# Optimization experiments

Hardware: AMD Instinct MI355X
Metric: run time of the kernel (lower is better)

The kernel has to match this reference:

```python
import jax, jax.numpy as jnp
import numpy as np
import math

B, L, S, T = 16, 256, 128, 128
Q_DIM, F_DIM, H_DIM, OUT_DIM = 512, 512, 512, 512


def setup_inputs() -> dict:
    key = jax.random.key(0)
    ks = jax.random.split(key, 10)
    inp = {
        "query": jax.random.normal(ks[0], (B, L, Q_DIM), dtype=jnp.float32),
        "src": jax.random.normal(ks[1], (B, S, F_DIM), dtype=jnp.float32),
        "trg": jax.random.normal(ks[2], (B, T, F_DIM), dtype=jnp.float32),
        # LinearAct params (Linear + identity act; out layer uses tanh)
        "Wq": jax.random.normal(ks[3], (Q_DIM, H_DIM), dtype=jnp.float32) / math.sqrt(Q_DIM),
        "bq": jnp.zeros((H_DIM,), dtype=jnp.float32),
        "Ws": jax.random.normal(ks[4], (F_DIM, H_DIM), dtype=jnp.float32) / math.sqrt(F_DIM),
        "bs": jnp.zeros((H_DIM,), dtype=jnp.float32),
        "Wt": jax.random.normal(ks[5], (F_DIM, H_DIM), dtype=jnp.float32) / math.sqrt(F_DIM),
        "bt": jnp.zeros((H_DIM,), dtype=jnp.float32),
        "Wo": jax.random.normal(ks[6], (2 * H_DIM + Q_DIM, OUT_DIM), dtype=jnp.float32) / math.sqrt(2 * H_DIM + Q_DIM),
        "bo": jnp.zeros((OUT_DIM,), dtype=jnp.float32),
    }
    return inp


def reference(query, src, trg, Wq, bq, Ws, bs, Wt, bt, Wo, bo):
    b, l, _ = query.shape
    _, s, f = src.shape
    _, t, _ = trg.shape
    hid_dim = Wq.shape[1]

    q = query @ Wq + bq                              # b, l, h
    # pad one all-zero feature row onto src and trg (as in torch.cat with pad_tensor)
    pad = jnp.zeros((b, 1, f), dtype=src.dtype)
    src_p = jnp.concatenate([src, pad], axis=1)       # b, s+1, f
    trg_p = jnp.concatenate([trg, pad], axis=1)       # b, t+1, f
    s_key = src_p @ Ws + bs                           # b, s+1, h
    t_key = trg_p @ Wt + bt                           # b, t+1, h

    # trilinear scores: b, l, s+1, t+1
    weight = jnp.einsum('blk,bsk,btk->blst', q, s_key, t_key) / math.sqrt(hid_dim)
    # joint softmax over the flattened (s+1)*(t+1) axis
    weight = jax.nn.softmax(weight.reshape(b, l, -1), axis=-1).reshape(b, l, s + 1, t + 1)

    s_ctx = jnp.einsum('blst,bsk->blk', weight, s_key)  # b, l, h
    t_ctx = jnp.einsum('blst,btk->blk', weight, t_key)  # b, l, h

    x = jnp.concatenate([query, s_ctx, t_ctx], axis=-1)  # b, l, q+2h
    return jnp.tanh(x @ Wo + bo)
```

## Files before the change

### kernel.cpp

```cpp
#include <hip/hip_runtime.h>
#include <math.h>

#define HD 512
#define SP 129
#define RPAD 144
#define WPAD 160
#define NBATCH 16
#define MQ 4096
#define SCALE 0.04419417382415922f
#define SCLG2E 0.06375871645788f
#define TANH2E 2.8853900817779268f

typedef _Float16 f16;
typedef _Float16 f16x8 __attribute__((ext_vector_type(8)));
typedef _Float16 f16x4 __attribute__((ext_vector_type(4)));
typedef float f32x4  __attribute__((ext_vector_type(4)));

__device__ __forceinline__ void gload_lds16(const f16* g, f16* l) {
  __builtin_amdgcn_global_load_lds(
      (const __attribute__((address_space(1))) void*)g,
      (__attribute__((address_space(3))) void*)l, 16, 0, 0);
}

__global__ __launch_bounds__(256) void prep_kernel(
    const float* __restrict__ Wq, const float* __restrict__ Ws,
    const float* __restrict__ Wt, const float* __restrict__ Wo,
    const float* __restrict__ bs, const float* __restrict__ bt,
    f16* __restrict__ WqT, f16* __restrict__ WsT,
    f16* __restrict__ WtT, f16* __restrict__ WoT,
    f16* __restrict__ skey, f16* __restrict__ tkey,
    f16* __restrict__ skeyT, f16* __restrict__ tkeyT)
{
  const int id = blockIdx.x;
  const int tid = threadIdx.x;
  if (id >= 384) {
    int i = (id - 384) * 256 + tid;
    int b = i >> 9, n = i & 511;
    for (int r = 128; r < RPAD; ++r) {
      skey[((size_t)b*RPAD + r)*HD + n] = (r == 128) ? (f16)bs[n] : (f16)0.f;
      tkey[((size_t)b*RPAD + r)*HD + n] = (r == 128) ? (f16)bt[n] : (f16)0.f;
    }
    size_t o = ((size_t)b*512 + n)*WPAD;
    for (int c = 128; c < WPAD; ++c) {
      skeyT[o + c] = (c == 128) ? (f16)bs[n] : (f16)0.f;
      tkeyT[o + c] = (c == 128) ? (f16)bt[n] : (f16)0.f;
    }
    return;
  }
  const float* W; f16* WT; int K; int rest;
  if (id < 64)       { W = Wq; WT = WqT; K = 512;  rest = id; }
  else if (id < 128) { W = Ws; WT = WsT; K = 512;  rest = id - 64; }
  else if (id < 192) { W = Wt; WT = WtT; K = 512;  rest = id - 128; }
  else               { W = Wo; WT = WoT; K = 1536; rest = id - 192; }
  const int k0 = (rest >> 3) * 64, n0 = (rest & 7) * 64;

  __shared__ float t[64][65];
  const int r = tid >> 4, c4 = (tid & 15) * 4;
  #pragma unroll
  for (int i = 0; i < 4; ++i) {
    int k = r + 16*i;
    float4 v = *(const float4*)(W + (size_t)(k0 + k)*512 + n0 + c4);
    t[k][c4] = v.x; t[k][c4+1] = v.y; t[k][c4+2] = v.z; t[k][c4+3] = v.w;
  }
  __syncthreads();
  #pragma unroll
  for (int i = 0; i < 4; ++i) {
    int n = r + 16*i;
    f16x4 v = { (f16)t[c4][n], (f16)t[c4+1][n], (f16)t[c4+2][n], (f16)t[c4+3][n] };
    *(f16x4*)(WT + (size_t)(n0 + n)*K + k0 + c4) = v;
  }
}

__global__ __launch_bounds__(256) void gemm_in(
    const float* __restrict__ query, const float* __restrict__ src,
    const float* __restrict__ trg,
    const f16* __restrict__ WqT, const f16* __restrict__ WsT,
    const f16* __restrict__ WtT,
    const float* __restrict__ bq, const float* __restrict__ bsv,
    const float* __restrict__ btv,
    f16* __restrict__ q_h, f16* __restrict__ skey, f16* __restrict__ tkey,
    f16* __restrict__ skeyT, f16* __restrict__ tkeyT)
{
  __shared__ __align__(16) f16 As[64*64];
  __shared__ __align__(16) f16 Bs[64*64];
  const int x = blockIdx.x;
  const float* A; const f16* WT; const float* bias; int bm; int iskey;
  f16 *Ch, *CT;
  if (x < 64)      { A = query; WT = WqT; bias = bq;  bm = x*64;      iskey = 0; Ch = q_h;  CT = nullptr; }
  else if (x < 96) { A = src;   WT = WsT; bias = bsv; bm = (x-64)*64; iskey = 1; Ch = skey; CT = skeyT; }
  else             { A = trg;   WT = WtT; bias = btv; bm = (x-96)*64; iskey = 1; Ch = tkey; CT = tkeyT; }
  const int bn = blockIdx.y * 64;
  const int tid  = threadIdx.x;
  const int lane = tid & 63;
  const int w    = tid >> 6;
  const int wr   = w & 1, wc = w >> 1;
  const int fq   = lane >> 4, fr = lane & 15;

  f32x4 acc[2][2] = {};

  for (int k0 = 0; k0 < 512; k0 += 64) {
    #pragma unroll
    for (int i = 0; i < 2; ++i) {
      int idx = tid + 256*i;
      int r = idx >> 3, c = idx & 7;
      const float* ap = A + (size_t)(bm + r)*512 + k0 + c*8;
      float4 x0 = *(const float4*)ap;
      float4 x1 = *(const float4*)(ap + 4);
      f16x8 va = { (f16)x0.x, (f16)x0.y, (f16)x0.z, (f16)x0.w,
                   (f16)x1.x, (f16)x1.y, (f16)x1.z, (f16)x1.w };
      const uint4 vb = *(const uint4*)(WT + (size_t)(bn + r)*512 + k0 + c*8);
      int o = ((r << 7) + (c << 4)) ^ ((r & 7) << 4);
      *(f16x8*)((char*)As + o) = va;
      *(uint4*)((char*)Bs + o) = vb;
    }
    __syncthreads();
    #pragma unroll
    for (int ks = 0; ks < 2; ++ks) {
      f16x8 af[2], bf_[2];
      #pragma unroll
      for (int i = 0; i < 2; ++i) {
        int ra = wr*32 + i*16 + fr;
        int oa = ((ra << 7) + (ks << 6) + (fq << 4)) ^ ((ra & 7) << 4);
        af[i] = *(const f16x8*)((const char*)As + oa);
        int rb = wc*32 + i*16 + fr;
        int ob = ((rb << 7) + (ks << 6) + (fq << 4)) ^ ((rb & 7) << 4);
        bf_[i] = *(const f16x8*)((const char*)Bs + ob);
      }
      #pragma unroll
      for (int i = 0; i < 2; ++i)
        #pragma unroll
        for (int j = 0; j < 2; ++j)
          acc[i][j] = __builtin_amdgcn_mfma_f32_16x16x32_f16(af[i], bf_[j], acc[i][j], 0, 0, 0);
    }
    __syncthreads();
  }

  #pragma unroll
  for (int i = 0; i < 2; ++i) {
    #pragma unroll
    for (int j = 0; j < 2; ++j) {
      int n = bn + wc*32 + j*16 + fr;
      float bv = bias[n];
      if (iskey) {
        const int m0 = bm + wr*32 + i*16 + fq*4;
        f16 vals[4];
        #pragma unroll
        for (int r = 0; r < 4; ++r) {
          int m = m0 + r;
          f16 xx = (f16)(acc[i][j][r] + bv);
          vals[r] = xx;
          int mo = (m >> 7) * RPAD + (m & 127);
          Ch[(size_t)mo*512 + n] = xx;
        }
        f16x4 v4 = { vals[0], vals[1], vals[2], vals[3] };
        *(f16x4*)(CT + ((size_t)(m0 >> 7)*512 + n)*WPAD + (m0 & 127)) = v4;
      } else {
        #pragma unroll
        for (int r = 0; r < 4; ++r) {
          int m = bm + wr*32 + i*16 + fq*4 + r;
          Ch[(size_t)m*512 + n] = (f16)(acc[i][j][r] + bv);
        }
      }
    }
  }
}

__global__ __launch_bounds__(256) void border_kernel(
    const f16* __restrict__ q_h, const f16* __restrict__ skey,
    const f16* __restrict__ tkey, float* __restrict__ Sb)
{
  const int blk = blockIdx.x;
  const int b  = blk >> 4;
  const int z  = (blk >> 3) & 1;
  const int mt = (blk >> 1) & 3;
  const int jh = blk & 1;
  const int j0 = jh ? 5 : 0;
  const int nj = jh ? 4 : 5;
  const int tasks = nj * 64;
  const f16* keys = (z ? skey : tkey) + ((size_t)b*RPAD + j0*16)*HD;
  const f16* u    = (z ? tkey : skey) + ((size_t)b*RPAD + 128)*HD;
  const int gid0 = b*256 + mt*64;

  __shared__ __align__(16) f16 Ks[80*32];
  const int tid = threadIdx.x, lane = tid & 63, w = tid >> 6;
  const int fq = lane >> 4, fr = lane & 15;
  const int rslot = (fq ^ ((fr >> 1) & 3)) * 8;

  f32x4 acc[5] = {};

  for (int kt = 0; kt < 16; ++kt) {
    uint4 t0, t1;
    {
      int r0 = tid >> 2, c0 = tid & 3;
      t0 = *(const uint4*)(keys + (size_t)r0*HD + kt*32 + c0*8);
      if (tid + 256 < tasks) {
        int r1 = (tid + 256) >> 2;
        t1 = *(const uint4*)(keys + (size_t)r1*HD + kt*32 + c0*8);
      }
    }
    __syncthreads();
    {
      int r0 = tid >> 2, c0 = tid & 3;
      int ws0 = (c0 ^ ((r0 >> 1) & 3)) * 8;
      *(uint4*)(&Ks[r0*32 + ws0]) = t0;
      if (tid + 256 < tasks) {
        int r1 = (tid + 256) >> 2;
        int ws1 = (c0 ^ ((r1 >> 1) & 3)) * 8;
        *(uint4*)(&Ks[r1*32 + ws1]) = t1;
      }
    }
    __syncthreads();
    const f16x8 qf = *(const f16x8*)(q_h + (size_t)(gid0 + w*16 + fr)*HD + kt*32 + fq*8);
    const f16x8 uv = *(const f16x8*)(u + kt*32 + fq*8);
    const f16x8 a = qf * uv;
    #pragma unroll
    for (int j = 0; j < 5; ++j) {
      if (j < nj) {
        const f16x8 bfr = *(const f16x8*)(&Ks[(j*16 + fr)*32 + rslot]);
        acc[j] = __builtin_amdgcn_mfma_f32_16x16x32_f16(a, bfr, acc[j], 0, 0, 0);
      }
    }
  }

  float* dst = Sb + (size_t)z*MQ*RPAD;
  #pragma unroll
  for (int j = 0; j < 5; ++j)
    if (j < nj) {
      #pragma unroll
      for (int r = 0; r < 4; ++r)
        dst[(size_t)(gid0 + w*16 + fq*4 + r)*RPAD + (j0 + j)*16 + fr] = acc[j][r];
    }
}

__global__ __launch_bounds__(256, 4) void attn_core(
    const f16* __restrict__ qg,
    const f16* __restrict__ skey,
    const f16* __restrict__ tkey,
    const float* __restrict__ Sb,
    f16* __restrict__ wsn,
    f16* __restrict__ wtn)
{
  __shared__ __align__(16) f16 KB[2*2*128*32];
  __shared__ __align__(16) f16 qs[HD];
  __shared__ float wsA[2][128];
  __shared__ float wtA[2][128];
  __shared__ float redA[4], redB[4], redC[4], redD[4], redE[4];
  __shared__ float cornerP;

  const int tid  = threadIdx.x;
  const int lane = tid & 63;
  const int w    = tid >> 6;
  const int rb   = w & 1;
  const int cb   = w >> 1;
  const int fq   = lane >> 4;
  const int fr   = lane & 15;
  const int so   = (fq ^ ((fr >> 1) & 3)) << 3;
  const int gc   = ((lane & 3) ^ ((lane >> 3) & 3)) * 8;

  const int gid = ((int)blockIdx.x & 7) * 512 + ((int)blockIdx.x >> 3);
  const int b   = gid >> 8;
  const f16* skg = skey + (size_t)b * RPAD * HD;
  const f16* tkg = tkey + (size_t)b * RPAD * HD;

  if (tid < 64) *(uint4*)(qs + tid*8) = *(const uint4*)(qg + (size_t)gid*HD + tid*8);

  auto stage = [&](int kt, int buf) {
    #pragma unroll
    for (int n = 0; n < 4; ++n) {
      int idx = w*4 + n;
      int key = idx >> 3;
      int rg  = idx & 7;
      const f16* g = (key ? tkg : skg)
                   + (size_t)(rg*16 + (lane >> 2))*HD + kt*32 + gc;
      f16* l = &KB[((buf*2 + key)*128 + rg*16)*32];
      gload_lds16(g, l);
    }
  };

  f32x4 acc[4][4] = {};

  auto mfma_kt = [&](int kt, int cur) {
    const f16x8 qv = *(const f16x8*)(&qs[kt*32 + fq*8]);
    const int abase = (cur*2 + 0)*128*32;
    const int bbase = (cur*2 + 1)*128*32;
    f16x8 B[4];
    #pragma unroll
    for (int j = 0; j < 4; ++j) {
      int rt = cb*64 + j*16 + fr;
      B[j] = *(const f16x8*)(&KB[bbase + rt*32 + so]);
    }
    __builtin_amdgcn_s_setprio(1);
    #pragma unroll
    for (int i = 0; i < 4; ++i) {
      int rs = rb*64 + i*16 + fr;
      const f16x8 raw = *(const f16x8*)(&KB[abase + rs*32 + so]);
      const f16x8 a = raw * qv;
      #pragma unroll
      for (int j = 0; j < 4; ++j)
        acc[i][j] = __builtin_amdgcn_mfma_f32_16x16x32_f16(a, B[j], acc[i][j], 0, 0, 0);
    }
    __builtin_amdgcn_s_setprio(0);
  };

  stage(0, 0);
  __syncthreads();

  for (int kt = 0; kt < 16; ++kt) {
    const int cur = kt & 1;
    if (kt < 15) {
      stage(kt + 1, cur ^ 1);
      asm volatile("s_waitcnt vmcnt(4)" ::: "memory");
    } else {
      asm volatile("s_waitcnt vmcnt(0)" ::: "memory");
    }
    __builtin_amdgcn_s_barrier();
    mfma_kt(kt, cur);
    __builtin_amdgcn_s_barrier();
  }

  float m = -3e38f;
  #pragma unroll
  for (int i = 0; i < 4; ++i)
    #pragma unroll
    for (int j = 0; j < 4; ++j)
      #pragma unroll
      for (int r = 0; r < 4; ++r) m = fmaxf(m, acc[i][j][r]);
  #pragma unroll
  for (int off = 32; off > 0; off >>= 1) m = fmaxf(m, __shfl_xor(m, off));
  if (lane == 0) redA[w] = m;

  const float* SbT = Sb + (size_t)gid*RPAD;
  const float* SbS = Sb + (size_t)MQ*RPAD + (size_t)gid*RPAD;
  const float btv = (tid < 129) ? SbT[tid] : -3e38f;
  const float bsv = (tid < 128) ? SbS[tid] : -3e38f;
  float bm = fmaxf(btv, bsv);
  #pragma unroll
  for (int off = 32; off > 0; off >>= 1) bm = fmaxf(bm, __shfl_xor(bm, off));
  if (lane == 0) redB[w] = bm;
  __syncthreads();
  const float mraw = fmaxf(
      fmaxf(fmaxf(redA[0], redA[1]), fmaxf(redA[2], redA[3])),
      fmaxf(fmaxf(redB[0], redB[1]), fmaxf(redB[2], redB[3])));

  float csum = 0.f;
  #pragma unroll
  for (int i = 0; i < 4; ++i)
    #pragma unroll
    for (int j = 0; j < 4; ++j)
      #pragma unroll
      for (int r = 0; r < 4; ++r) {
        float p = exp2f((acc[i][j][r] - mraw) * SCLG2E);
        acc[i][j][r] = p;
        csum += p;
      }
  #pragma unroll
  for (int off = 32; off > 0; off >>= 1) csum += __shfl_xor(csum, off);
  if (lane == 0) redC[w] = csum;

  #pragma unroll
  for (int i = 0; i < 4; ++i) {
    #pragma unroll
    for (int r = 0; r < 4; ++r) {
      float rs = acc[i][0][r] + acc[i][1][r] + acc[i][2][r] + acc[i][3][r];
      rs += __shfl_xor(rs, 1); rs += __shfl_xor(rs, 2);
      rs += __shfl_xor(rs, 4); rs += __shfl_xor(rs, 8);
      if (fr == 0) wsA[cb][rb*64 + i*16 + fq*4 + r] = rs;
    }
  }
  #pragma unroll
  for (int j = 0; j < 4; ++j) {
    float cs = 0.f;
    #pragma unroll
    for (int i = 0; i < 4; ++i)
      #pragma unroll
      for (int r = 0; r < 4; ++r) cs += acc[i][j][r];
    cs += __shfl_xor(cs, 16); cs += __shfl_xor(cs, 32);
    if (fq == 0) wtA[rb][cb*64 + j*16 + fr] = cs;
  }

  const float pbt = (tid < 129) ? exp2f((btv - mraw) * SCLG2E) : 0.f;
  const float pbs = (tid < 128) ? exp2f((bsv - mraw) * SCLG2E) : 0.f;
  float sbt = pbt, sbs = pbs;
  #pragma unroll
  for (int off = 32; off > 0; off >>= 1) {
    sbt += __shfl_xor(sbt, off);
    sbs += __shfl_xor(sbs, off);
  }
  if (lane == 0) { redD[w] = sbt; redE[w] = sbs; }
  if (tid == 128) cornerP = pbt;
  __syncthreads();

  const float pbt_sum = redD[0] + redD[1] + redD[2] + redD[3];
  const float pbs_sum = redE[0] + redE[1] + redE[2] + redE[3];
  const float core_sum = redC[0] + redC[1] + redC[2] + redC[3];
  const float invZ = 1.0f / (core_sum + pbt_sum + pbs_sum);

  if (tid < WPAD) {
    float wsv = (tid < 128) ? (wsA[0][tid] + wsA[1][tid] + pbs)
              : (tid == 128) ? pbt_sum : 0.f;
    float wtv = (tid < 128) ? (wtA[0][tid] + wtA[1][tid] + pbt)
              : (tid == 128) ? (pbs_sum + cornerP) : 0.f;
    wsn[(size_t)gid*WPAD + tid] = (f16)(wsv * invZ);
    wtn[(size_t)gid*WPAD + tid] = (f16)(wtv * invZ);
  }
}

__global__ __launch_bounds__(256) void ctx_gemm(
    const f16* __restrict__ wsn, const f16* __restrict__ wtn,
    const f16* __restrict__ skeyT, const f16* __restrict__ tkeyT,
    f16* __restrict__ sctx, f16* __restrict__ tctx)
{
  __shared__ __align__(16) f16 As[64*168];
  __shared__ __align__(16) f16 Bs[64*168];
  const int z = blockIdx.x & 1, b = blockIdx.x >> 1;
  const int mt = blockIdx.y, nt = blockIdx.z;
  const int tid = threadIdx.x, lane = tid & 63, w = tid >> 6;
  const int wr = w & 1, wc = w >> 1;
  const int fq = lane >> 4, fr = lane & 15;

  const f16* A  = (z ? wtn : wsn) + ((size_t)b*256 + mt*64)*WPAD;
  const f16* Bt = (z ? tkeyT : skeyT) + ((size_t)b*512 + nt*64)*WPAD;

  for (int t = tid; t < 1280; t += 256) {
    int r = t / 20, c = t % 20;
    *(uint4*)(&As[r*168 + c*8]) = *(const uint4*)(A + (size_t)r*WPAD + c*8);
    *(uint4*)(&Bs[r*168 + c*8]) = *(const uint4*)(Bt + (size_t)r*WPAD + c*8);
  }
  __syncthreads();

  f32x4 acc[2][2] = {};
  #pragma unroll
  for (int ks = 0; ks < 5; ++ks) {
    f16x8 af[2], bf_[2];
    #pragma unroll
    for (int i = 0; i < 2; ++i) {
      af[i]  = *(const f16x8*)(&As[(wr*32 + i*16 + fr)*168 + ks*32 + fq*8]);
      bf_[i] = *(const f16x8*)(&Bs[(wc*32 + i*16 + fr)*168 + ks*32 + fq*8]);
    }
    #pragma unroll
    for (int i = 0; i < 2; ++i)
      #pragma unroll
      for (int j = 0; j < 2; ++j)
        acc[i][j] = __builtin_amdgcn_mfma_f32_16x16x32_f16(af[i], bf_[j], acc[i][j], 0, 0, 0);
  }

  f16* out = z ? tctx : sctx;
  #pragma unroll
  for (int i = 0; i < 2; ++i)
    #pragma unroll
    for (int j = 0; j < 2; ++j) {
      int col = nt*64 + wc*32 + j*16 + fr;
      #pragma unroll
      for (int r = 0; r < 4; ++r) {
        int row = b*256 + mt*64 + wr*32 + i*16 + fq*4 + r;
        out[(size_t)row*HD + col] = (f16)acc[i][j][r];
      }
    }
}

__global__ __launch_bounds__(256) void gemm_out(
    const float* __restrict__ query, const f16* __restrict__ sctx,
    const f16* __restrict__ tctx, const f16* __restrict__ WoT,
    const float* __restrict__ bias, float* __restrict__ C)
{
  __shared__ __align__(16) f16 As[64*64];
  __shared__ __align__(16) f16 Bs[64*64];
  const int tid  = threadIdx.x;
  const int lane = tid & 63;
  const int w    = tid >> 6;
  const int wr   = w & 1, wc = w >> 1;
  const int fq   = lane >> 4, fr = lane & 15;
  const int bm = blockIdx.x * 64, bn = blockIdx.y * 64;

  f32x4 acc[2][2] = {};

  for (int k0 = 0; k0 < 1536; k0 += 64) {
    const int seg  = k0 >> 9;
    const int kloc = k0 & 511;
    #pragma unroll
    for (int i = 0; i < 2; ++i) {
      int idx = tid + 256*i;
      int r = idx >> 3, c = idx & 7;
      int o = ((r << 7) + (c << 4)) ^ ((r & 7) << 4);
      if (seg == 0) {
        const float* ap = query + (size_t)(bm + r)*512 + kloc + c*8;
        float4 x0 = *(const float4*)ap;
        float4 x1 = *(const float4*)(ap + 4);
        f16x8 va = { (f16)x0.x, (f16)x0.y, (f16)x0.z, (f16)x0.w,
                     (f16)x1.x, (f16)x1.y, (f16)x1.z, (f16)x1.w };
        *(f16x8*)((char*)As + o) = va;
      } else {
        const f16* Ap = (seg == 1) ? sctx : tctx;
        *(uint4*)((char*)As + o) = *(const uint4*)(Ap + (size_t)(bm + r)*512 + kloc + c*8);
      }
      *(uint4*)((char*)Bs + o) = *(const uint4*)(WoT + (size_t)(bn + r)*1536 + k0 + c*8);
    }
    __syncthreads();
    #pragma unroll
    for (int ks = 0; ks < 2; ++ks) {
      f16x8 af[2], bf_[2];
      #pragma unroll
      for (int i = 0; i < 2; ++i) {
        int ra = wr*32 + i*16 + fr;
        int oa = ((ra << 7) + (ks << 6) + (fq << 4)) ^ ((ra & 7) << 4);
        af[i] = *(const f16x8*)((const char*)As + oa);
        int rb = wc*32 + i*16 + fr;
        int ob = ((rb << 7) + (ks << 6) + (fq << 4)) ^ ((rb & 7) << 4);
        bf_[i] = *(const f16x8*)((const char*)Bs + ob);
      }
      #pragma unroll
      for (int i = 0; i < 2; ++i)
        #pragma unroll
        for (int j = 0; j < 2; ++j)
          acc[i][j] = __builtin_amdgcn_mfma_f32_16x16x32_f16(af[i], bf_[j], acc[i][j], 0, 0, 0);
    }
    __syncthreads();
  }

  #pragma unroll
  for (int i = 0; i < 2; ++i)
    #pragma unroll
    for (int j = 0; j < 2; ++j) {
      int n = bn + wc*32 + j*16 + fr;
      float bv = bias[n];
      #pragma unroll
      for (int r = 0; r < 4; ++r) {
        int m = bm + wr*32 + i*16 + fq*4 + r;
        float xx = acc[i][j][r] + bv;
        xx = fminf(fmaxf(xx, -20.f), 20.f);
        float e = exp2f(TANH2E * xx);
        C[(size_t)m*HD + n] = (e - 1.0f) / (e + 1.0f);
      }
    }
}

extern "C" void kernel_launch(void* const* d_in, const int* in_sizes, int n_in,
                              void* d_out, int out_size, void* d_ws, size_t ws_size,
                              hipStream_t stream) {
  (void)in_sizes; (void)n_in; (void)out_size; (void)ws_size;
  const float* query = (const float*)d_in[0];
  const float* src   = (const float*)d_in[1];
  const float* trg   = (const float*)d_in[2];
  const float* Wq    = (const float*)d_in[3];
  const float* bq    = (const float*)d_in[4];
  const float* Wsm   = (const float*)d_in[5];
  const float* bs    = (const float*)d_in[6];
  const float* Wtm   = (const float*)d_in[7];
  const float* bt    = (const float*)d_in[8];
  const float* Wo    = (const float*)d_in[9];
  const float* bo    = (const float*)d_in[10];
  float* out = (float*)d_out;

  char* p = (char*)d_ws;
  f16* WqT   = (f16*)p;  p += (size_t)HD*HD*2;
  f16* WsT   = (f16*)p;  p += (size_t)HD*HD*2;
  f16* WtT   = (f16*)p;  p += (size_t)HD*HD*2;
  f16* WoT   = (f16*)p;  p += (size_t)1536*HD*2;
  f16* q_h   = (f16*)p;  p += (size_t)MQ*HD*2;
  f16* skey  = (f16*)p;  p += (size_t)NBATCH*RPAD*HD*2;
  f16* tkey  = (f16*)p;  p += (size_t)NBATCH*RPAD*HD*2;
  f16* skeyT = (f16*)p;  p += (size_t)NBATCH*HD*WPAD*2;
  f16* tkeyT = (f16*)p;  p += (size_t)NBATCH*HD*WPAD*2;
  f16* wsn   = (f16*)p;  p += (size_t)MQ*WPAD*2;
  f16* wtn   = (f16*)p;  p += (size_t)MQ*WPAD*2;
  f16* sctx  = (f16*)p;  p += (size_t)MQ*HD*2;
  f16* tctx  = (f16*)p;  p += (size_t)MQ*HD*2;
  float* Sb  = (float*)p; p += (size_t)2*MQ*RPAD*4;

  dim3 blk(256);
  prep_kernel<<<dim3(416), blk, 0, stream>>>(Wq, Wsm, Wtm, Wo, bs, bt,
                                             WqT, WsT, WtT, WoT,
                                             skey, tkey, skeyT, tkeyT);
  gemm_in<<<dim3(128, 8), blk, 0, stream>>>(query, src, trg, WqT, WsT, WtT,
                                            bq, bs, bt, q_h, skey, tkey,
                                            skeyT, tkeyT);
  border_kernel<<<dim3(256), blk, 0, stream>>>(q_h, skey, tkey, Sb);
  attn_core<<<dim3(MQ), blk, 0, stream>>>(q_h, skey, tkey, Sb, wsn, wtn);
  ctx_gemm<<<dim3(32, 4, 8), blk, 0, stream>>>(wsn, wtn, skeyT, tkeyT, sctx, tctx);
  gemm_out<<<dim3(64, 8), blk, 0, stream>>>(query, sctx, tctx, WoT, bo, out);
}
```

Measured before the change: 192.3 us.

## Replace per-row attention blocks with persistent key-resident quadrant blocks plus combine

Each of 256 persistent blocks now loads one 64x64 quadrant of source and target keys (about 128 KB) into LDS once. Its four waves then process 64 query rows against those resident keys. Before, each of 4096 blocks streamed all keys through double-buffered LDS. A separate combine kernel adds the quadrant partial row and column sums, adds the border terms and normalises. The running-max subtraction is dropped, so exp2 is taken on raw scores, and the partial sums reuse the sctx/tctx buffers as scratch. The trade-off is occupancy of one block per CU with only four waves to hide latency, and possible overflow for larger score magnitudes.

```diff
diff --git a/kernel.cpp b/kernel.cpp
--- a/kernel.cpp
+++ b/kernel.cpp
@@ -232,176 +232,149 @@
     }
 }
 
-__global__ __launch_bounds__(256, 4) void attn_core(
+__global__ __launch_bounds__(256, 1) void attn_persist(
     const f16* __restrict__ qg,
     const f16* __restrict__ skey,
     const f16* __restrict__ tkey,
+    float* __restrict__ pws,
+    float* __restrict__ pwt)
+{
+  __shared__ __align__(16) f16 KS[64*512];
+  __shared__ __align__(16) f16 KT[64*512];
+  const int tid = threadIdx.x, lane = tid & 63, w = tid >> 6;
+  const int fq = lane >> 4, fr = lane & 15;
+
+  const int blk = ((int)blockIdx.x & 7) * 32 + ((int)blockIdx.x >> 3);
+  const int b  = blk >> 4;
+  const int qd = (blk >> 2) & 3;
+  const int sh = qd >> 1, th = qd & 1;
+  const int rg = blk & 3;
+  const f16* skg = skey + ((size_t)b*RPAD + sh*64)*HD;
+  const f16* tkg = tkey + ((size_t)b*RPAD + th*64)*HD;
+
+  const int lgrp = (lane >> 3) * 8;
+  const int llow = lane & 7;
+  for (int n = 0; n < 32; ++n) {
+    int idx = w*32 + n;
+    int key = idx >> 6;
+    int r = idx & 63;
+    const f16* gb = key ? tkg : skg;
+    const f16* g = gb + (size_t)r*HD + (lgrp + (llow ^ (r & 7)))*8;
+    f16* l = (key ? KT : KS) + r*512;
+    gload_lds16(g, l);
+  }
+  asm volatile("s_waitcnt vmcnt(0)" ::: "memory");
+  __syncthreads();
+
+  for (int rr = 0; rr < 16; ++rr) {
+    const int gid = b*256 + rg*64 + w*16 + rr;
+    const f16* qrow = qg + (size_t)gid*HD;
+    f16x8 qbuf[16];
+    #pragma unroll
+    for (int kt = 0; kt < 16; ++kt)
+      qbuf[kt] = *(const f16x8*)(qrow + kt*32 + fq*8);
+
+    f32x4 acc[4][4] = {};
+    #pragma unroll
+    for (int kt = 0; kt < 16; ++kt) {
+      const int cbase = kt*4 + fq;
+      const int cgrp  = cbase & 56;
+      const int clow  = cbase & 7;
+      f16x8 B[4];
+      #pragma unroll
+      for (int j = 0; j < 4; ++j) {
+        int rt = j*16 + fr;
+        int p = cgrp | (clow ^ (rt & 7));
+        B[j] = *(const f16x8*)(KT + rt*512 + p*8);
+      }
+      __builtin_amdgcn_s_setprio(1);
+      #pragma unroll
+      for (int i = 0; i < 4; ++i) {
+        int rs = i*16 + fr;
+        int p = cgrp | (clow ^ (rs & 7));
+        const f16x8 raw = *(const f16x8*)(KS + rs*512 + p*8);
+        const f16x8 a = raw * qbuf[kt];
+        #pragma unroll
+        for (int j = 0; j < 4; ++j)
+          acc[i][j] = __builtin_amdgcn_mfma_f32_16x16x32_f16(a, B[j], acc[i][j], 0, 0, 0);
+      }
+      __builtin_amdgcn_s_setprio(0);
+    }
+
+    #pragma unroll
+    for (int i = 0; i < 4; ++i)
+      #pragma unroll
+      for (int j = 0; j < 4; ++j)
+        #pragma unroll
+        for (int r = 0; r < 4; ++r)
+          acc[i][j][r] = exp2f(acc[i][j][r] * SCLG2E);
+
+    #pragma unroll
+    for (int i = 0; i < 4; ++i) {
+      #pragma unroll
+      for (int r = 0; r < 4; ++r) {
+        float rs = acc[i][0][r] + acc[i][1][r] + acc[i][2][r] + acc[i][3][r];
+        rs += __shfl_xor(rs, 1); rs += __shfl_xor(rs, 2);
+        rs += __shfl_xor(rs, 4); rs += __shfl_xor(rs, 8);
+        if (fr == 0)
+          pws[((size_t)gid*2 + th)*128 + sh*64 + i*16 + fq*4 + r] = rs;
+      }
+    }
+    #pragma unroll
+    for (int j = 0; j < 4; ++j) {
+      float cs = 0.f;
+      #pragma unroll
+      for (int i = 0; i < 4; ++i)
+        #pragma unroll
+        for (int r = 0; r < 4; ++r) cs += acc[i][j][r];
+      cs += __shfl_xor(cs, 16); cs += __shfl_xor(cs, 32);
+      if (fq == 0)
+        pwt[((size_t)gid*2 + sh)*128 + th*64 + j*16 + fr] = cs;
+    }
+  }
+}
+
+__global__ __launch_bounds__(256) void combine_kernel(
+    const float* __restrict__ pws, const float* __restrict__ pwt,
     const float* __restrict__ Sb,
-    f16* __restrict__ wsn,
-    f16* __restrict__ wtn)
-{
-  __shared__ __align__(16) f16 KB[2*2*128*32];
-  __shared__ __align__(16) f16 qs[HD];
-  __shared__ float wsA[2][128];
-  __shared__ float wtA[2][128];
-  __shared__ float redA[4], redB[4], redC[4], redD[4], redE[4];
+    f16* __restrict__ wsn, f16* __restrict__ wtn)
+{
+  __shared__ float redZ[4], redT[4], redS[4];
   __shared__ float cornerP;
-
-  const int tid  = threadIdx.x;
-  const int lane = tid & 63;
-  const int w    = tid >> 6;
-  const int rb   = w & 1;
-  const int cb   = w >> 1;
-  const int fq   = lane >> 4;
-  const int fr   = lane & 15;
-  const int so   = (fq ^ ((fr >> 1) & 3)) << 3;
-  const int gc   = ((lane & 3) ^ ((lane >> 3) & 3)) * 8;
-
-  const int gid = ((int)blockIdx.x & 7) * 512 + ((int)blockIdx.x >> 3);
-  const int b   = gid >> 8;
-  const f16* skg = skey + (size_t)b * RPAD * HD;
-  const f16* tkg = tkey + (size_t)b * RPAD * HD;
-
-  if (tid < 64) *(uint4*)(qs + tid*8) = *(const uint4*)(qg + (size_t)gid*HD + tid*8);
-
-  auto stage = [&](int kt, int buf) {
-    #pragma unroll
-    for (int n = 0; n < 4; ++n) {
-      int idx = w*4 + n;
-      int key = idx >> 3;
-      int rg  = idx & 7;
-      const f16* g = (key ? tkg : skg)
-                   + (size_t)(rg*16 + (lane >> 2))*HD + kt*32 + gc;
-      f16* l = &KB[((buf*2 + key)*128 + rg*16)*32];
-      gload_lds16(g, l);
-    }
-  };
-
-  f32x4 acc[4][4] = {};
-
-  auto mfma_kt = [&](int kt, int cur) {
-    const f16x8 qv = *(const f16x8*)(&qs[kt*32 + fq*8]);
-    const int abase = (cur*2 + 0)*128*32;
-    const int bbase = (cur*2 + 1)*128*32;
-    f16x8 B[4];
-    #pragma unroll
-    for (int j = 0; j < 4; ++j) {
-      int rt = cb*64 + j*16 + fr;
-      B[j] = *(const f16x8*)(&KB[bbase + rt*32 + so]);
-    }
-    __builtin_amdgcn_s_setprio(1);
-    #pragma unroll
-    for (int i = 0; i < 4; ++i) {
-      int rs = rb*64 + i*16 + fr;
-      const f16x8 raw = *(const f16x8*)(&KB[abase + rs*32 + so]);
-      const f16x8 a = raw * qv;
-      #pragma unroll
-      for (int j = 0; j < 4; ++j)
-        acc[i][j] = __builtin_amdgcn_mfma_f32_16x16x32_f16(a, B[j], acc[i][j], 0, 0, 0);
-    }
-    __builtin_amdgcn_s_setprio(0);
-  };
-
-  stage(0, 0);
-  __syncthreads();
-
-  for (int kt = 0; kt < 16; ++kt) {
-    const int cur = kt & 1;
-    if (kt < 15) {
-      stage(kt + 1, cur ^ 1);
-      asm volatile("s_waitcnt vmcnt(4)" ::: "memory");
-    } else {
-      asm volatile("s_waitcnt vmcnt(0)" ::: "memory");
-    }
-    __builtin_amdgcn_s_barrier();
-    mfma_kt(kt, cur);
-    __builtin_amdgcn_s_barrier();
-  }
-
-  float m = -3e38f;
-  #pragma unroll
-  for (int i = 0; i < 4; ++i)
-    #pragma unroll
-    for (int j = 0; j < 4; ++j)
-      #pragma unroll
-      for (int r = 0; r < 4; ++r) m = fmaxf(m, acc[i][j][r]);
-  #pragma unroll
-  for (int off = 32; off > 0; off >>= 1) m = fmaxf(m, __shfl_xor(m, off));
-  if (lane == 0) redA[w] = m;
-
-  const float* SbT = Sb + (size_t)gid*RPAD;
-  const float* SbS = Sb + (size_t)MQ*RPAD + (size_t)gid*RPAD;
-  const float btv = (tid < 129) ? SbT[tid] : -3e38f;
-  const float bsv = (tid < 128) ? SbS[tid] : -3e38f;
-  float bm = fmaxf(btv, bsv);
-  #pragma unroll
-  for (int off = 32; off > 0; off >>= 1) bm = fmaxf(bm, __shfl_xor(bm, off));
-  if (lane == 0) redB[w] = bm;
-  __syncthreads();
-  const float mraw = fmaxf(
-      fmaxf(fmaxf(redA[0], redA[1]), fmaxf(redA[2], redA[3])),
-      fmaxf(fmaxf(redB[0], redB[1]), fmaxf(redB[2], redB[3])));
-
-  float csum = 0.f;
-  #pragma unroll
-  for (int i = 0; i < 4; ++i)
-    #pragma unroll
-    for (int j = 0; j < 4; ++j)
-      #pragma unroll
-      for (int r = 0; r < 4; ++r) {
-        float p = exp2f((acc[i][j][r] - mraw) * SCLG2E);
-        acc[i][j][r] = p;
-        csum += p;
-      }
-  #pragma unroll
-  for (int off = 32; off > 0; off >>= 1) csum += __shfl_xor(csum, off);
-  if (lane == 0) redC[w] = csum;
-
-  #pragma unroll
-  for (int i = 0; i < 4; ++i) {
-    #pragma unroll
-    for (int r = 0; r < 4; ++r) {
-      float rs = acc[i][0][r] + acc[i][1][r] + acc[i][2][r] + acc[i][3][r];
-      rs += __shfl_xor(rs, 1); rs += __shfl_xor(rs, 2);
-      rs += __shfl_xor(rs, 4); rs += __shfl_xor(rs, 8);
-      if (fr == 0) wsA[cb][rb*64 + i*16 + fq*4 + r] = rs;
-    }
-  }
-  #pragma unroll
-  for (int j = 0; j < 4; ++j) {
-    float cs = 0.f;
-    #pragma unroll
-    for (int i = 0; i < 4; ++i)
-      #pragma unroll
-      for (int r = 0; r < 4; ++r) cs += acc[i][j][r];
-    cs += __shfl_xor(cs, 16); cs += __shfl_xor(cs, 32);
-    if (fq == 0) wtA[rb][cb*64 + j*16 + fr] = cs;
-  }
-
-  const float pbt = (tid < 129) ? exp2f((btv - mraw) * SCLG2E) : 0.f;
-  const float pbs = (tid < 128) ? exp2f((bsv - mraw) * SCLG2E) : 0.f;
-  float sbt = pbt, sbs = pbs;
-  #pragma unroll
-  for (int off = 32; off > 0; off >>= 1) {
-    sbt += __shfl_xor(sbt, off);
-    sbs += __shfl_xor(sbs, off);
-  }
-  if (lane == 0) { redD[w] = sbt; redE[w] = sbs; }
-  if (tid == 128) cornerP = pbt;
-  __syncthreads();
-
-  const float pbt_sum = redD[0] + redD[1] + redD[2] + redD[3];
-  const float pbs_sum = redE[0] + redE[1] + redE[2] + redE[3];
-  const float core_sum = redC[0] + redC[1] + redC[2] + redC[3];
-  const float invZ = 1.0f / (core_sum + pbt_sum + pbs_sum);
-
-  if (tid < WPAD) {
-    float wsv = (tid < 128) ? (wsA[0][tid] + wsA[1][tid] + pbs)
-              : (tid == 128) ? pbt_sum : 0.f;
-    float wtv = (tid < 128) ? (wtA[0][tid] + wtA[1][tid] + pbt)
-              : (tid == 128) ? (pbs_sum + cornerP) : 0.f;
-    wsn[(size_t)gid*WPAD + tid] = (f16)(wsv * invZ);
-    wtn[(size_t)gid*WPAD + tid] = (f16)(wtv * invZ);
+  const int tid = threadIdx.x, lane = tid & 63, w = tid >> 6;
+
+  for (int rr = 0; rr < 16; ++rr) {
+    const int gid = blockIdx.x * 16 + rr;
+    const float* SbT = Sb + (size_t)gid*RPAD;
+    const float* SbS = Sb + (size_t)MQ*RPAD + (size_t)gid*RPAD;
+    const float pbt = (tid < 129) ? exp2f(SbT[tid]*SCLG2E) : 0.f;
+    const float pbs = (tid < 128) ? exp2f(SbS[tid]*SCLG2E) : 0.f;
+    float wsc = 0.f, wtc = 0.f;
+    if (tid < 128) {
+      wsc = pws[((size_t)gid*2 + 0)*128 + tid] + pws[((size_t)gid*2 + 1)*128 + tid];
+      wtc = pwt[((size_t)gid*2 + 0)*128 + tid] + pwt[((size_t)gid*2 + 1)*128 + tid];
+    }
+    float zc = wsc, zt = pbt, zs = pbs;
+    #pragma unroll
+    for (int off = 32; off > 0; off >>= 1) {
+      zc += __shfl_xor(zc, off);
+      zt += __shfl_xor(zt, off);
+      zs += __shfl_xor(zs, off);
+    }
+    if (lane == 0) { redZ[w] = zc; redT[w] = zt; redS[w] = zs; }
+    if (tid == 128) cornerP = pbt;
+    __syncthreads();
+    const float wsc_sum = redZ[0] + redZ[1] + redZ[2] + redZ[3];
+    const float pbt_sum = redT[0] + redT[1] + redT[2] + redT[3];
+    const float pbs_sum = redS[0] + redS[1] + redS[2] + redS[3];
+    const float invZ = 1.0f / (wsc_sum + pbt_sum + pbs_sum);
+    if (tid < WPAD) {
+      float wsv = (tid < 128) ? (wsc + pbs) : (tid == 128) ? pbt_sum : 0.f;
+      float wtv = (tid < 128) ? (wtc + pbt) : (tid == 128) ? (pbs_sum + cornerP) : 0.f;
+      wsn[(size_t)gid*WPAD + tid] = (f16)(wsv * invZ);
+      wtn[(size_t)gid*WPAD + tid] = (f16)(wtv * invZ);
+    }
+    __syncthreads();
   }
 }
 
@@ -566,6 +539,8 @@
   f16* sctx  = (f16*)p;  p += (size_t)MQ*HD*2;
   f16* tctx  = (f16*)p;  p += (size_t)MQ*HD*2;
   float* Sb  = (float*)p; p += (size_t)2*MQ*RPAD*4;
+  float* pws = (float*)sctx;
+  float* pwt = (float*)tctx;
 
   dim3 blk(256);
   prep_kernel<<<dim3(416), blk, 0, stream>>>(Wq, Wsm, Wtm, Wo, bs, bt,
@@ -575,7 +550,8 @@
                                             bq, bs, bt, q_h, skey, tkey,
                                             skeyT, tkeyT);
   border_kernel<<<dim3(256), blk, 0, stream>>>(q_h, skey, tkey, Sb);
-  attn_core<<<dim3(MQ), blk, 0, stream>>>(q_h, skey, tkey, Sb, wsn, wtn);
+  attn_persist<<<dim3(256), blk, 0, stream>>>(q_h, skey, tkey, pws, pwt);
+  combine_kernel<<<dim3(256), blk, 0, stream>>>(pws, pwt, Sb, wsn, wtn);
   ctx_gemm<<<dim3(32, 4, 8), blk, 0, stream>>>(wsn, wtn, skeyT, tkeyT, sctx, tctx);
   gemm_out<<<dim3(64, 8), blk, 0, stream>>>(query, sctx, tctx, WoT, bo, out);
 }
```

After: 229.7 us. 1.19x slower.
